# Optimization experiments

Hardware: AMD Instinct MI355X
Metric: run time of the kernel (lower is better)

## Reference

```python
import jax, jax.numpy as jnp
import numpy as np


def _pair_indices(num_emb):
    # pair (i, j), i != j; torch builds pair vector = concat(emb[j], emb[i])
    ii, jj = np.meshgrid(np.arange(num_emb), np.arange(num_emb), indexing='ij')
    mask = ii != jj
    return jnp.asarray(ii[mask]), jnp.asarray(jj[mask])


def setup_inputs() -> dict:
    key = jax.random.key(0)
    ks = jax.random.split(key, 8)
    B, n_way, n_shot, n_query, F = 64, 2, 6, 16, 512
    s = 0.02
    return {
        'x_shot_feat': jax.random.normal(ks[0], (B * n_way * n_shot, F), jnp.float32),
        'x_query_feat': jax.random.normal(ks[1], (B * n_query, F), jnp.float32),
        'Wg1': jax.random.normal(ks[2], (2 * F, F), jnp.float32) * s,
        'bg1': jnp.zeros((F,), jnp.float32),
        'Wg2': jax.random.normal(ks[3], (F, F), jnp.float32) * s,
        'bg2': jnp.zeros((F,), jnp.float32),
        'Wf1': jax.random.normal(ks[4], (F, F), jnp.float32) * s,
        'bf1': jnp.zeros((F,), jnp.float32),
        'Wf2': jax.random.normal(ks[5], (F, 1), jnp.float32) * s,
        'bf2': jnp.zeros((1,), jnp.float32),
        'batch_size': B, 'n_way': n_way, 'n_shot': n_shot, 'n_query': n_query,
    }


def reference(x_shot_feat, x_query_feat, Wg1, bg1, Wg2, bg2, Wf1, bf1, Wf2, bf2,
              batch_size, n_way, n_shot, n_query):
    F = x_shot_feat.shape[-1]
    num_emb = n_shot + 1
    x_shot = x_shot_feat.reshape(batch_size, n_way, n_shot, F)
    pos, neg = x_shot[:, 0], x_shot[:, 1]          # [B, n_shot, F]
    q = x_query_feat.reshape(batch_size, n_query, F)

    # emb: [B, Q, way=2, num_emb, F]  (support set + the single query appended)
    shot = jnp.stack([pos, neg], axis=1)           # [B, 2, n_shot, F]
    shot_b = jnp.broadcast_to(shot[:, None], (batch_size, n_query, 2, n_shot, F))
    q_b = jnp.broadcast_to(q[:, :, None, None, :], (batch_size, n_query, 2, 1, F))
    emb = jnp.concatenate([shot_b, q_b], axis=3)   # [B, Q, 2, num_emb, F]

    idx_i, idx_j = _pair_indices(num_emb)          # P = num_emb^2 - num_emb
    # pair(i,j) = concat(emb[j], emb[i])  (matches torch expand order)
    pairs = jnp.concatenate([emb[..., idx_j, :], emb[..., idx_i, :]], axis=-1)  # [B,Q,2,P,2F]

    g = jax.nn.relu(pairs @ Wg1 + bg1)
    g = jax.nn.relu(g @ Wg2 + bg2)                 # [B, Q, 2, P, F]
    s = jnp.sum(g, axis=3)                         # [B, Q, 2, F]
    logit = jax.nn.relu(s @ Wf1 + bf1) @ Wf2 + bf2 # [B, Q, 2, 1]
    return logit[..., 0]                           # [B, Q, n_way]
```

## Files before the change

### kernel.cpp

```cpp
#include <hip/hip_runtime.h>
#include <stdint.h>

typedef _Float16 f16x8 __attribute__((ext_vector_type(8)));
typedef float f32x4 __attribute__((ext_vector_type(4)));

__device__ __forceinline__ void gload16(const void* g, void* l) {
  __builtin_amdgcn_global_load_lds((const __attribute__((address_space(1))) void*)g,
                                   (__attribute__((address_space(3))) void*)l,
                                   16, 0, 0);
}

__device__ __forceinline__ void maprow_ss(int gr, int& rowU, int& rowV, bool& ok) {
  int g = gr >> 5, p = gr & 31;
  ok = (p < 30);
  int i = p / 5, jj = p % 5;
  int j = jj + (jj >= i);
  rowU = g * 6 + j;
  rowV = g * 6 + i;
  if (!ok) { rowU = 0; rowV = 0; }
}

__device__ __forceinline__ void maprow_sq(int gr, int& rowU, int& rowV) {
  int h = gr / 12, p = gr % 12;
  int b = h >> 5, q = (h >> 1) & 15, wv = h & 1;
  int sbase = (b * 2 + wv) * 6;
  int qrow = 768 + b * 16 + q;
  if (p < 6) { rowU = qrow; rowV = sbase + p; }
  else       { rowU = sbase + (p - 6); rowV = qrow; }
}

__device__ __forceinline__ f16x8 cvt8h(float4 a, float4 b) {
  f16x8 o;
  o[0] = (_Float16)a.x; o[1] = (_Float16)a.y; o[2] = (_Float16)a.z; o[3] = (_Float16)a.w;
  o[4] = (_Float16)b.x; o[5] = (_Float16)b.y; o[6] = (_Float16)b.z; o[7] = (_Float16)b.w;
  return o;
}

__global__ void convert_t(const float* __restrict__ Wg1, const float* __restrict__ Wg2,
                          const float* __restrict__ Wf1, const float* __restrict__ bf2,
                          _Float16* __restrict__ Wg1T, _Float16* __restrict__ Wg2T,
                          _Float16* __restrict__ Wf1T, float* __restrict__ out) {
  int tt = blockIdx.x * 256 + threadIdx.x;
  if (tt < 2048) out[tt] = bf2[0];
  const float* src;
  _Float16* dst;
  int c, k0, scol, srow0;
  if (tt < 65536) {
    c = tt & 1023; k0 = (tt >> 10) << 3;
    dst = Wg1T + (size_t)c * 512 + k0;
    if (c < 512) { src = Wg1; scol = c; srow0 = k0; }
    else         { src = Wg1; scol = c - 512; srow0 = 512 + k0; }
  } else if (tt < 98304) {
    int t2 = tt - 65536;
    c = t2 & 511; k0 = (t2 >> 9) << 3;
    dst = Wg2T + (size_t)c * 512 + k0;
    src = Wg2; scol = c; srow0 = k0;
  } else {
    int t3 = tt - 98304;
    c = t3 & 511; k0 = (t3 >> 9) << 3;
    dst = Wf1T + (size_t)c * 512 + k0;
    src = Wf1; scol = c; srow0 = k0;
  }
  f16x8 o;
#pragma unroll
  for (int i = 0; i < 8; i++)
    o[i] = (_Float16)src[(size_t)(srow0 + i) * 512 + scol];
  *(f16x8*)dst = o;
}

__global__ __launch_bounds__(256, 2) void gemm1_fused(
    const float* __restrict__ xs, const float* __restrict__ xq,
    const _Float16* __restrict__ BT, const float* __restrict__ bg1,
    _Float16* __restrict__ UVh) {
  __shared__ __align__(16) char smem[16384];

  int bid = blockIdx.x;
  { int q = gridDim.x >> 3; bid = (bid & 7) * q + (bid >> 3); }
  const int tm = bid >> 4;
  const int tn = bid & 15;
  const int t = threadIdx.x, w = t >> 6, l = t & 63;
  const int wm = (w >> 1) << 5, wn = (w & 1) << 5;
  const int lr = l & 15, lg = l >> 4;

  const int rl0 = t >> 2, c = t & 3;
  const int wchunk = c ^ ((rl0 >> 2) & 3);
  const int gr0 = tm * 64 + rl0;
  const float* x0 = ((gr0 < 768) ? xs + (size_t)gr0 * 512 : xq + (size_t)(gr0 - 768) * 512) + c * 8;

  const int kch = ((t & 3) ^ ((t >> 4) & 3)) * 8;
  const _Float16* Bg = BT + (size_t)(tn * 64 + rl0) * 512 + kch;

  _Float16* As_base = (_Float16*)smem;
  char*     Bs_base = smem + 8192;

  f32x4 acc[2][2];
#pragma unroll
  for (int m = 0; m < 2; m++)
#pragma unroll
    for (int n = 0; n < 2; n++) acc[m][n] = (f32x4){0.f, 0.f, 0.f, 0.f};
  const int rchunk = (lg ^ (lr >> 2)) * 8;

  gload16(Bg, Bs_base + t * 16);
  {
    float4 a0 = *(const float4*)(x0), a1 = *(const float4*)(x0 + 4);
    *(f16x8*)(As_base + rl0 * 32 + wchunk * 8) = cvt8h(a0, a1);
  }
  __syncthreads();

  int cur = 0;
  for (int it = 0; it < 15; ++it) {
    const int nxt = cur ^ 1;
    const int kn = (it + 1) * 32;
    gload16(Bg + kn, Bs_base + nxt * 4096 + t * 16);
    float4 a0 = *(const float4*)(x0 + kn), a1 = *(const float4*)(x0 + kn + 4);
    {
      _Float16* As = As_base + cur * 2048;
      _Float16* Bs = (_Float16*)(Bs_base + cur * 4096);
      f16x8 fa[2], fb[2];
#pragma unroll
      for (int m = 0; m < 2; m++)
        fa[m] = *(const f16x8*)(As + (wm + m * 16 + lr) * 32 + rchunk);
#pragma unroll
      for (int n = 0; n < 2; n++)
        fb[n] = *(const f16x8*)(Bs + (wn + n * 16 + lr) * 32 + rchunk);
#pragma unroll
      for (int m = 0; m < 2; m++)
#pragma unroll
        for (int n = 0; n < 2; n++)
          acc[m][n] = __builtin_amdgcn_mfma_f32_16x16x32_f16(fa[m], fb[n], acc[m][n], 0, 0, 0);
    }
    *(f16x8*)(As_base + nxt * 2048 + rl0 * 32 + wchunk * 8) = cvt8h(a0, a1);
    __syncthreads();
    cur = nxt;
  }
  {
    _Float16* As = As_base + cur * 2048;
    _Float16* Bs = (_Float16*)(Bs_base + cur * 4096);
    f16x8 fa[2], fb[2];
#pragma unroll
    for (int m = 0; m < 2; m++)
      fa[m] = *(const f16x8*)(As + (wm + m * 16 + lr) * 32 + rchunk);
#pragma unroll
    for (int n = 0; n < 2; n++)
      fb[n] = *(const f16x8*)(Bs + (wn + n * 16 + lr) * 32 + rchunk);
#pragma unroll
    for (int m = 0; m < 2; m++)
#pragma unroll
      for (int n = 0; n < 2; n++)
        acc[m][n] = __builtin_amdgcn_mfma_f32_16x16x32_f16(fa[m], fb[n], acc[m][n], 0, 0, 0);
  }

#pragma unroll
  for (int m = 0; m < 2; m++)
#pragma unroll
    for (int n = 0; n < 2; n++) {
      int col = tn * 64 + wn + n * 16 + lr;
      float bv = (col >= 512) ? bg1[col - 512] : 0.0f;
#pragma unroll
      for (int reg = 0; reg < 4; reg++) {
        int row = tm * 64 + wm + m * 16 + lg * 4 + reg;
        UVh[(size_t)row * 1024 + col] = (_Float16)(acc[m][n][reg] + bv);
      }
    }
}

__global__ __launch_bounds__(256, 2) void gemm2_fused(
    const _Float16* __restrict__ UVh,
    const _Float16* __restrict__ BT, const float* __restrict__ bg2,
    float* __restrict__ outSS, float* __restrict__ outSQ) {
  __shared__ __align__(16) char smem[24576];

  int bid = blockIdx.x;
  { int q = gridDim.x >> 3; bid = (bid & 7) * q + (bid >> 3); }
  const int t = threadIdx.x, w = t >> 6, l = t & 63;
  const int lr = l & 15, lg = l >> 4;
  const int rl = t >> 2, c = t & 3;
  const int wchunk = c ^ ((t >> 4) & 3);
  const int kch = ((t & 3) ^ ((t >> 4) & 3)) * 8;
  const int rchunk = (lg ^ (lr >> 2)) * 8;
  const f16x8 zz = {};
  char* Bsb = smem + 16384;

  if (bid < 2048) {
    const int tile = bid >> 3, tn = bid & 7;
    const int wm = (w >> 1) * 48, wn = (w & 1) << 5;

    int rU0, rV0, rU1 = 0, rV1 = 0;
    maprow_sq(tile * 96 + rl, rU0, rV0);
    if (t < 128) maprow_sq(tile * 96 + 64 + rl, rU1, rV1);
    const _Float16* u0p = UVh + (size_t)rU0 * 1024 + c * 8;
    const _Float16* v0p = UVh + (size_t)rV0 * 1024 + 512 + c * 8;
    const _Float16* u1p = UVh + (size_t)rU1 * 1024 + c * 8;
    const _Float16* v1p = UVh + (size_t)rV1 * 1024 + 512 + c * 8;
    const _Float16* Bg = BT + (size_t)(tn * 64 + rl) * 512 + kch;

    f32x4 acc[3][2];
#pragma unroll
    for (int m = 0; m < 3; m++)
#pragma unroll
      for (int n = 0; n < 2; n++) acc[m][n] = (f32x4){0.f, 0.f, 0.f, 0.f};

    {
      f16x8 u0 = *(const f16x8*)(u0p), v0 = *(const f16x8*)(v0p);
      *(f16x8*)((_Float16*)smem + rl * 32 + wchunk * 8) =
          __builtin_elementwise_max(u0 + v0, zz);
      if (t < 128) {
        f16x8 u1 = *(const f16x8*)(u1p), v1 = *(const f16x8*)(v1p);
        *(f16x8*)((_Float16*)smem + (64 + rl) * 32 + wchunk * 8) =
            __builtin_elementwise_max(u1 + v1, zz);
      }
    }
    gload16(Bg, Bsb + t * 16);
    __syncthreads();

    int cur = 0;
    for (int it = 0; it < 15; ++it) {
      const int nxt = cur ^ 1;
      const int kn = (it + 1) * 32;
      gload16(Bg + kn, Bsb + nxt * 4096 + t * 16);
      f16x8 u0 = *(const f16x8*)(u0p + kn), v0 = *(const f16x8*)(v0p + kn);
      f16x8 u1, v1;
      if (t < 128) { u1 = *(const f16x8*)(u1p + kn); v1 = *(const f16x8*)(v1p + kn); }
      {
        _Float16* As = (_Float16*)(smem + cur * 6144);
        _Float16* Bs = (_Float16*)(Bsb + cur * 4096);
        f16x8 fa[3], fb[2];
#pragma unroll
        for (int m = 0; m < 3; m++)
          fa[m] = *(const f16x8*)(As + (wm + m * 16 + lr) * 32 + rchunk);
#pragma unroll
        for (int n = 0; n < 2; n++)
          fb[n] = *(const f16x8*)(Bs + (wn + n * 16 + lr) * 32 + rchunk);
#pragma unroll
        for (int m = 0; m < 3; m++)
#pragma unroll
          for (int n = 0; n < 2; n++)
            acc[m][n] = __builtin_amdgcn_mfma_f32_16x16x32_f16(fa[m], fb[n], acc[m][n], 0, 0, 0);
      }
      {
        _Float16* Aw = (_Float16*)(smem + nxt * 6144);
        *(f16x8*)(Aw + rl * 32 + wchunk * 8) = __builtin_elementwise_max(u0 + v0, zz);
        if (t < 128)
          *(f16x8*)(Aw + (64 + rl) * 32 + wchunk * 8) = __builtin_elementwise_max(u1 + v1, zz);
      }
      __syncthreads();
      cur = nxt;
    }
    {
      _Float16* As = (_Float16*)(smem + cur * 6144);
      _Float16* Bs = (_Float16*)(Bsb + cur * 4096);
      f16x8 fa[3], fb[2];
#pragma unroll
      for (int m = 0; m < 3; m++)
        fa[m] = *(const f16x8*)(As + (wm + m * 16 + lr) * 32 + rchunk);
#pragma unroll
      for (int n = 0; n < 2; n++)
        fb[n] = *(const f16x8*)(Bs + (wn + n * 16 + lr) * 32 + rchunk);
#pragma unroll
      for (int m = 0; m < 3; m++)
#pragma unroll
        for (int n = 0; n < 2; n++)
          acc[m][n] = __builtin_amdgcn_mfma_f32_16x16x32_f16(fa[m], fb[n], acc[m][n], 0, 0, 0);
    }
    __syncthreads();

    float* scr = (float*)smem + w * 192;
#pragma unroll
    for (int n = 0; n < 2; n++) {
      int col = tn * 64 + wn + n * 16 + lr;
      float bv = bg2[col];
#pragma unroll
      for (int m = 0; m < 3; m++) {
        float s = 0.0f;
#pragma unroll
        for (int reg = 0; reg < 4; reg++)
          s += fmaxf(acc[m][n][reg] + bv, 0.0f);
        scr[(4 * m + lg) * 16 + lr] = s;
      }
#pragma unroll
      for (int g = 0; g < 4; g++) {
        float vs = scr[(3 * g) * 16 + lr] + scr[(3 * g + 1) * 16 + lr] +
                   scr[(3 * g + 2) * 16 + lr];
        if (l < 16) {
          int hh = tile * 8 + ((wm == 48) ? 4 : 0) + g;
          outSQ[(size_t)hh * 512 + col] = vs;
        }
      }
    }
  } else {
    const int sbid = bid - 2048;
    const int tm = sbid >> 3, tn = sbid & 7;
    const int wm = (w >> 1) << 6, wn = (w & 1) << 5;

    int rU0, rV0, rU1, rV1; bool ok0, ok1;
    maprow_ss(tm * 128 + rl, rU0, rV0, ok0);
    maprow_ss(tm * 128 + rl + 64, rU1, rV1, ok1);
    const _Float16* u0p = UVh + (size_t)rU0 * 1024 + c * 8;
    const _Float16* v0p = UVh + (size_t)rV0 * 1024 + 512 + c * 8;
    const _Float16* u1p = UVh + (size_t)rU1 * 1024 + c * 8;
    const _Float16* v1p = UVh + (size_t)rV1 * 1024 + 512 + c * 8;
    const _Float16* Bg = BT + (size_t)(tn * 64 + rl) * 512 + kch;

    f32x4 acc[4][2];
#pragma unroll
    for (int m = 0; m < 4; m++)
#pragma unroll
      for (int n = 0; n < 2; n++) acc[m][n] = (f32x4){0.f, 0.f, 0.f, 0.f};

    {
      f16x8 u0 = *(const f16x8*)(u0p), v0 = *(const f16x8*)(v0p);
      f16x8 u1 = *(const f16x8*)(u1p), v1 = *(const f16x8*)(v1p);
      f16x8 o0 = ok0 ? __builtin_elementwise_max(u0 + v0, zz) : zz;
      f16x8 o1 = ok1 ? __builtin_elementwise_max(u1 + v1, zz) : zz;
      *(f16x8*)((_Float16*)smem + rl * 32 + wchunk * 8) = o0;
      *(f16x8*)((_Float16*)smem + (rl + 64) * 32 + wchunk * 8) = o1;
    }
    gload16(Bg, Bsb + t * 16);
    __syncthreads();

    int cur = 0;
    for (int it = 0; it < 15; ++it) {
      const int nxt = cur ^ 1;
      const int kn = (it + 1) * 32;
      gload16(Bg + kn, Bsb + nxt * 4096 + t * 16);
      f16x8 u0 = *(const f16x8*)(u0p + kn), v0 = *(const f16x8*)(v0p + kn);
      f16x8 u1 = *(const f16x8*)(u1p + kn), v1 = *(const f16x8*)(v1p + kn);
      {
        _Float16* As = (_Float16*)(smem + cur * 8192);
        _Float16* Bs = (_Float16*)(Bsb + cur * 4096);
        f16x8 fa[4], fb[2];
#pragma unroll
        for (int m = 0; m < 4; m++)
          fa[m] = *(const f16x8*)(As + (wm + m * 16 + lr) * 32 + rchunk);
#pragma unroll
        for (int n = 0; n < 2; n++)
          fb[n] = *(const f16x8*)(Bs + (wn + n * 16 + lr) * 32 + rchunk);
#pragma unroll
        for (int m = 0; m < 4; m++)
#pragma unroll
          for (int n = 0; n < 2; n++)
            acc[m][n] = __builtin_amdgcn_mfma_f32_16x16x32_f16(fa[m], fb[n], acc[m][n], 0, 0, 0);
      }
      {
        f16x8 o0 = ok0 ? __builtin_elementwise_max(u0 + v0, zz) : zz;
        f16x8 o1 = ok1 ? __builtin_elementwise_max(u1 + v1, zz) : zz;
        _Float16* Aw = (_Float16*)(smem + nxt * 8192);
        *(f16x8*)(Aw + rl * 32 + wchunk * 8) = o0;
        *(f16x8*)(Aw + (rl + 64) * 32 + wchunk * 8) = o1;
      }
      __syncthreads();
      cur = nxt;
    }
    {
      _Float16* As = (_Float16*)(smem + cur * 8192);
      _Float16* Bs = (_Float16*)(Bsb + cur * 4096);
      f16x8 fa[4], fb[2];
#pragma unroll
      for (int m = 0; m < 4; m++)
        fa[m] = *(const f16x8*)(As + (wm + m * 16 + lr) * 32 + rchunk);
#pragma unroll
      for (int n = 0; n < 2; n++)
        fb[n] = *(const f16x8*)(Bs + (wn + n * 16 + lr) * 32 + rchunk);
#pragma unroll
      for (int m = 0; m < 4; m++)
#pragma unroll
        for (int n = 0; n < 2; n++)
          acc[m][n] = __builtin_amdgcn_mfma_f32_16x16x32_f16(fa[m], fb[n], acc[m][n], 0, 0, 0);
    }

#pragma unroll
    for (int pair = 0; pair < 2; pair++) {
#pragma unroll
      for (int n = 0; n < 2; n++) {
        int col = tn * 64 + wn + n * 16 + lr;
        float bv = bg2[col];
        float s = 0.0f;
#pragma unroll
        for (int mh = 0; mh < 2; mh++) {
          int m = pair * 2 + mh;
#pragma unroll
          for (int reg = 0; reg < 4; reg++) {
            bool ok = (mh == 0) || (lg * 4 + reg < 14);
            float v = fmaxf(acc[m][n][reg] + bv, 0.0f);
            s += ok ? v : 0.0f;
          }
        }
        s += __shfl_xor(s, 16);
        s += __shfl_xor(s, 32);
        if (l < 16) {
          int g = (wm >> 5) + pair;
          outSS[(size_t)(tm * 4 + g) * 512 + col] = s;
        }
      }
    }
  }
}

__global__ __launch_bounds__(256, 2) void gemm3_fused(
    const float* __restrict__ SS, const float* __restrict__ SQ,
    const _Float16* __restrict__ BT, const float* __restrict__ bf1,
    const float* __restrict__ Wf2, float* __restrict__ out) {
  __shared__ __align__(16) char smem[16384];

  int bid = blockIdx.x;
  { int q = gridDim.x >> 3; bid = (bid & 7) * q + (bid >> 3); }
  const int tm = bid >> 3;
  const int tn = bid & 7;
  const int t = threadIdx.x, w = t >> 6, l = t & 63;
  const int wm = (w >> 1) << 5, wn = (w & 1) << 5;
  const int lr = l & 15, lg = l >> 4;

  const int rl0 = t >> 2, c = t & 3;
  const int wchunk = c ^ ((rl0 >> 2) & 3);
  const int gr0 = tm * 64 + rl0;
  const int ss0 = (gr0 >> 5) * 2 + (gr0 & 1);
  const float* s0p = SS + (size_t)ss0 * 512 + c * 8;
  const float* q0p = SQ + (size_t)gr0 * 512 + c * 8;

  const int kch = ((t & 3) ^ ((t >> 4) & 3)) * 8;
  const _Float16* Bg = BT + (size_t)(tn * 64 + rl0) * 512 + kch;

  _Float16* As_base = (_Float16*)smem;
  char*     Bs_base = smem + 8192;

  f32x4 acc[2][2];
#pragma unroll
  for (int m = 0; m < 2; m++)
#pragma unroll
    for (int n = 0; n < 2; n++) acc[m][n] = (f32x4){0.f, 0.f, 0.f, 0.f};
  const int rchunk = (lg ^ (lr >> 2)) * 8;

#define BUILD_S(o, a0, a1, b0, b1)                                           \
  {                                                                          \
    o[0] = (_Float16)(a0.x + b0.x); o[1] = (_Float16)(a0.y + b0.y);          \
    o[2] = (_Float16)(a0.z + b0.z); o[3] = (_Float16)(a0.w + b0.w);          \
    o[4] = (_Float16)(a1.x + b1.x); o[5] = (_Float16)(a1.y + b1.y);          \
    o[6] = (_Float16)(a1.z + b1.z); o[7] = (_Float16)(a1.w + b1.w);          \
  }

  gload16(Bg, Bs_base + t * 16);
  {
    float4 a0 = *(const float4*)(s0p), a1 = *(const float4*)(s0p + 4);
    float4 b0 = *(const float4*)(q0p), b1 = *(const float4*)(q0p + 4);
    f16x8 o0;
    BUILD_S(o0, a0, a1, b0, b1);
    *(f16x8*)(As_base + rl0 * 32 + wchunk * 8) = o0;
  }
  __syncthreads();

  int cur = 0;
  for (int it = 0; it < 15; ++it) {
    const int nxt = cur ^ 1;
    const int kn = (it + 1) * 32;
    gload16(Bg + kn, Bs_base + nxt * 4096 + t * 16);
    float4 a0 = *(const float4*)(s0p + kn), a1 = *(const float4*)(s0p + kn + 4);
    float4 b0 = *(const float4*)(q0p + kn), b1 = *(const float4*)(q0p + kn + 4);
    {
      _Float16* As = As_base + cur * 2048;
      _Float16* Bs = (_Float16*)(Bs_base + cur * 4096);
      f16x8 fa[2], fb[2];
#pragma unroll
      for (int m = 0; m < 2; m++)
        fa[m] = *(const f16x8*)(As + (wm + m * 16 + lr) * 32 + rchunk);
#pragma unroll
      for (int n = 0; n < 2; n++)
        fb[n] = *(const f16x8*)(Bs + (wn + n * 16 + lr) * 32 + rchunk);
#pragma unroll
      for (int m = 0; m < 2; m++)
#pragma unroll
        for (int n = 0; n < 2; n++)
          acc[m][n] = __builtin_amdgcn_mfma_f32_16x16x32_f16(fa[m], fb[n], acc[m][n], 0, 0, 0);
    }
    {
      f16x8 o0;
      BUILD_S(o0, a0, a1, b0, b1);
      *(f16x8*)(As_base + nxt * 2048 + rl0 * 32 + wchunk * 8) = o0;
    }
    __syncthreads();
    cur = nxt;
  }
  {
    _Float16* As = As_base + cur * 2048;
    _Float16* Bs = (_Float16*)(Bs_base + cur * 4096);
    f16x8 fa[2], fb[2];
#pragma unroll
    for (int m = 0; m < 2; m++)
      fa[m] = *(const f16x8*)(As + (wm + m * 16 + lr) * 32 + rchunk);
#pragma unroll
    for (int n = 0; n < 2; n++)
      fb[n] = *(const f16x8*)(Bs + (wn + n * 16 + lr) * 32 + rchunk);
#pragma unroll
    for (int m = 0; m < 2; m++)
#pragma unroll
      for (int n = 0; n < 2; n++)
        acc[m][n] = __builtin_amdgcn_mfma_f32_16x16x32_f16(fa[m], fb[n], acc[m][n], 0, 0, 0);
  }

  float bf1v[2], wf2v[2];
#pragma unroll
  for (int n = 0; n < 2; n++) {
    int col = tn * 64 + wn + n * 16 + lr;
    bf1v[n] = bf1[col];
    wf2v[n] = Wf2[col];
  }
#pragma unroll
  for (int m = 0; m < 2; m++) {
#pragma unroll
    for (int reg = 0; reg < 4; reg++) {
      float p = 0.0f;
#pragma unroll
      for (int n = 0; n < 2; n++)
        p += fmaxf(acc[m][n][reg] + bf1v[n], 0.0f) * wf2v[n];
      p += __shfl_xor(p, 1);
      p += __shfl_xor(p, 2);
      p += __shfl_xor(p, 4);
      p += __shfl_xor(p, 8);
      if (lr == 0) {
        int row = tm * 64 + wm + m * 16 + lg * 4 + reg;
        atomicAdd(&out[row], p);
      }
    }
  }
#undef BUILD_S
}

extern "C" void kernel_launch(void* const* d_in, const int* in_sizes, int n_in,
                              void* d_out, int out_size, void* d_ws, size_t ws_size,
                              hipStream_t stream) {
  const float* xs  = (const float*)d_in[0];
  const float* xq  = (const float*)d_in[1];
  const float* Wg1 = (const float*)d_in[2];
  const float* bg1 = (const float*)d_in[3];
  const float* Wg2 = (const float*)d_in[4];
  const float* bg2 = (const float*)d_in[5];
  const float* Wf1 = (const float*)d_in[6];
  const float* bf1 = (const float*)d_in[7];
  const float* Wf2 = (const float*)d_in[8];
  const float* bf2 = (const float*)d_in[9];
  float* out = (float*)d_out;

  char* ws = (char*)d_ws;
  _Float16* Wg1T = (_Float16*)(ws);
  _Float16* Wg2T = (_Float16*)(ws + 1048576);
  _Float16* Wf1T = (_Float16*)(ws + 1572864);
  _Float16* UVh  = (_Float16*)(ws + 2097152);
  float*    SSs  = (float*)(ws + 5767168);
  float*    SQs  = (float*)(ws + 6029312);

  convert_t<<<512, 256, 0, stream>>>(Wg1, Wg2, Wf1, bf2, Wg1T, Wg2T, Wf1T, out);
  gemm1_fused<<<448, 256, 0, stream>>>(xs, xq, Wg1T, bg1, UVh);
  gemm2_fused<<<2304, 256, 0, stream>>>(UVh, Wg2T, bg2, SSs, SQs);
  gemm3_fused<<<256, 256, 0, stream>>>(SSs, SQs, Wf1T, bf1, Wf2, out);
}
```

Before: 64.14 us.

## Widen gemm2 tiles to 128 columns with 512-thread blocks

Doubles the N-tile width of the fused second GEMM from 64 to 128 columns and runs it with 8 waves per 512-thread block, halving the grid. Each block now builds its relu(U+V) A-tile once per 128 output columns instead of once per 64, so the pair-gather and add work and the UVh reads are cut in half. The B shared buffer doubles and the block shrinks to one per CU by launch bounds, which may lower latency hiding and occupancy.

```diff
diff --git a/kernel.cpp b/kernel.cpp
--- a/kernel.cpp
+++ b/kernel.cpp
@@ -164,35 +164,34 @@
     }
 }
 
-__global__ __launch_bounds__(256, 2) void gemm2_fused(
+__global__ __launch_bounds__(512, 1) void gemm2_fused(
     const _Float16* __restrict__ UVh,
     const _Float16* __restrict__ BT, const float* __restrict__ bg2,
     float* __restrict__ outSS, float* __restrict__ outSQ) {
-  __shared__ __align__(16) char smem[24576];
+  __shared__ __align__(16) char smem[32768];
 
   int bid = blockIdx.x;
   { int q = gridDim.x >> 3; bid = (bid & 7) * q + (bid >> 3); }
   const int t = threadIdx.x, w = t >> 6, l = t & 63;
   const int lr = l & 15, lg = l >> 4;
   const int rl = t >> 2, c = t & 3;
-  const int wchunk = c ^ ((t >> 4) & 3);
+  const int wchunk = c ^ ((rl >> 2) & 3);
   const int kch = ((t & 3) ^ ((t >> 4) & 3)) * 8;
   const int rchunk = (lg ^ (lr >> 2)) * 8;
   const f16x8 zz = {};
   char* Bsb = smem + 16384;
 
-  if (bid < 2048) {
-    const int tile = bid >> 3, tn = bid & 7;
-    const int wm = (w >> 1) * 48, wn = (w & 1) << 5;
-
-    int rU0, rV0, rU1 = 0, rV1 = 0;
-    maprow_sq(tile * 96 + rl, rU0, rV0);
-    if (t < 128) maprow_sq(tile * 96 + 64 + rl, rU1, rV1);
+  if (bid < 1024) {
+    const int tile = bid >> 2, tn = bid & 3;
+    const int wm = (w >> 2) * 48;
+    const int wn = (w & 3) << 5;
+    const bool st = (t < 384);
+
+    int rU0 = 0, rV0 = 0;
+    if (st) maprow_sq(tile * 96 + rl, rU0, rV0);
     const _Float16* u0p = UVh + (size_t)rU0 * 1024 + c * 8;
     const _Float16* v0p = UVh + (size_t)rV0 * 1024 + 512 + c * 8;
-    const _Float16* u1p = UVh + (size_t)rU1 * 1024 + c * 8;
-    const _Float16* v1p = UVh + (size_t)rV1 * 1024 + 512 + c * 8;
-    const _Float16* Bg = BT + (size_t)(tn * 64 + rl) * 512 + kch;
+    const _Float16* Bg = BT + (size_t)(tn * 128 + rl) * 512 + kch;
 
     f32x4 acc[3][2];
 #pragma unroll
@@ -200,15 +199,10 @@
 #pragma unroll
       for (int n = 0; n < 2; n++) acc[m][n] = (f32x4){0.f, 0.f, 0.f, 0.f};
 
-    {
+    if (st) {
       f16x8 u0 = *(const f16x8*)(u0p), v0 = *(const f16x8*)(v0p);
       *(f16x8*)((_Float16*)smem + rl * 32 + wchunk * 8) =
           __builtin_elementwise_max(u0 + v0, zz);
-      if (t < 128) {
-        f16x8 u1 = *(const f16x8*)(u1p), v1 = *(const f16x8*)(v1p);
-        *(f16x8*)((_Float16*)smem + (64 + rl) * 32 + wchunk * 8) =
-            __builtin_elementwise_max(u1 + v1, zz);
-      }
     }
     gload16(Bg, Bsb + t * 16);
     __syncthreads();
@@ -217,13 +211,12 @@
     for (int it = 0; it < 15; ++it) {
       const int nxt = cur ^ 1;
       const int kn = (it + 1) * 32;
-      gload16(Bg + kn, Bsb + nxt * 4096 + t * 16);
-      f16x8 u0 = *(const f16x8*)(u0p + kn), v0 = *(const f16x8*)(v0p + kn);
-      f16x8 u1, v1;
-      if (t < 128) { u1 = *(const f16x8*)(u1p + kn); v1 = *(const f16x8*)(v1p + kn); }
+      gload16(Bg + kn, Bsb + nxt * 8192 + t * 16);
+      f16x8 u0, v0;
+      if (st) { u0 = *(const f16x8*)(u0p + kn); v0 = *(const f16x8*)(v0p + kn); }
       {
         _Float16* As = (_Float16*)(smem + cur * 6144);
-        _Float16* Bs = (_Float16*)(Bsb + cur * 4096);
+        _Float16* Bs = (_Float16*)(Bsb + cur * 8192);
         f16x8 fa[3], fb[2];
 #pragma unroll
         for (int m = 0; m < 3; m++)
@@ -237,18 +230,16 @@
           for (int n = 0; n < 2; n++)
             acc[m][n] = __builtin_amdgcn_mfma_f32_16x16x32_f16(fa[m], fb[n], acc[m][n], 0, 0, 0);
       }
-      {
+      if (st) {
         _Float16* Aw = (_Float16*)(smem + nxt * 6144);
         *(f16x8*)(Aw + rl * 32 + wchunk * 8) = __builtin_elementwise_max(u0 + v0, zz);
-        if (t < 128)
-          *(f16x8*)(Aw + (64 + rl) * 32 + wchunk * 8) = __builtin_elementwise_max(u1 + v1, zz);
       }
       __syncthreads();
       cur = nxt;
     }
     {
       _Float16* As = (_Float16*)(smem + cur * 6144);
-      _Float16* Bs = (_Float16*)(Bsb + cur * 4096);
+      _Float16* Bs = (_Float16*)(Bsb + cur * 8192);
       f16x8 fa[3], fb[2];
 #pragma unroll
       for (int m = 0; m < 3; m++)
@@ -267,7 +258,7 @@
     float* scr = (float*)smem + w * 192;
 #pragma unroll
     for (int n = 0; n < 2; n++) {
-      int col = tn * 64 + wn + n * 16 + lr;
+      int col = tn * 128 + wn + n * 16 + lr;
       float bv = bg2[col];
 #pragma unroll
       for (int m = 0; m < 3; m++) {
@@ -288,18 +279,16 @@
       }
     }
   } else {
-    const int sbid = bid - 2048;
-    const int tm = sbid >> 3, tn = sbid & 7;
-    const int wm = (w >> 1) << 6, wn = (w & 1) << 5;
-
-    int rU0, rV0, rU1, rV1; bool ok0, ok1;
+    const int sbid = bid - 1024;
+    const int tm = sbid >> 2, tn = sbid & 3;
+    const int wm = (w >> 2) << 6;
+    const int wn = (w & 3) << 5;
+
+    int rU0, rV0; bool ok0;
     maprow_ss(tm * 128 + rl, rU0, rV0, ok0);
-    maprow_ss(tm * 128 + rl + 64, rU1, rV1, ok1);
     const _Float16* u0p = UVh + (size_t)rU0 * 1024 + c * 8;
     const _Float16* v0p = UVh + (size_t)rV0 * 1024 + 512 + c * 8;
-    const _Float16* u1p = UVh + (size_t)rU1 * 1024 + c * 8;
-    const _Float16* v1p = UVh + (size_t)rV1 * 1024 + 512 + c * 8;
-    const _Float16* Bg = BT + (size_t)(tn * 64 + rl) * 512 + kch;
+    const _Float16* Bg = BT + (size_t)(tn * 128 + rl) * 512 + kch;
 
     f32x4 acc[4][2];
 #pragma unroll
@@ -309,11 +298,8 @@
 
     {
       f16x8 u0 = *(const f16x8*)(u0p), v0 = *(const f16x8*)(v0p);
-      f16x8 u1 = *(const f16x8*)(u1p), v1 = *(const f16x8*)(v1p);
       f16x8 o0 = ok0 ? __builtin_elementwise_max(u0 + v0, zz) : zz;
-      f16x8 o1 = ok1 ? __builtin_elementwise_max(u1 + v1, zz) : zz;
       *(f16x8*)((_Float16*)smem + rl * 32 + wchunk * 8) = o0;
-      *(f16x8*)((_Float16*)smem + (rl + 64) * 32 + wchunk * 8) = o1;
     }
     gload16(Bg, Bsb + t * 16);
     __syncthreads();
@@ -322,12 +308,11 @@
     for (int it = 0; it < 15; ++it) {
       const int nxt = cur ^ 1;
       const int kn = (it + 1) * 32;
-      gload16(Bg + kn, Bsb + nxt * 4096 + t * 16);
+      gload16(Bg + kn, Bsb + nxt * 8192 + t * 16);
       f16x8 u0 = *(const f16x8*)(u0p + kn), v0 = *(const f16x8*)(v0p + kn);
-      f16x8 u1 = *(const f16x8*)(u1p + kn), v1 = *(const f16x8*)(v1p + kn);
       {
         _Float16* As = (_Float16*)(smem + cur * 8192);
-        _Float16* Bs = (_Float16*)(Bsb + cur * 4096);
+        _Float16* Bs = (_Float16*)(Bsb + cur * 8192);
         f16x8 fa[4], fb[2];
 #pragma unroll
         for (int m = 0; m < 4; m++)
@@ -343,17 +328,15 @@
       }
       {
         f16x8 o0 = ok0 ? __builtin_elementwise_max(u0 + v0, zz) : zz;
-        f16x8 o1 = ok1 ? __builtin_elementwise_max(u1 + v1, zz) : zz;
         _Float16* Aw = (_Float16*)(smem + nxt * 8192);
         *(f16x8*)(Aw + rl * 32 + wchunk * 8) = o0;
-        *(f16x8*)(Aw + (rl + 64) * 32 + wchunk * 8) = o1;
       }
       __syncthreads();
       cur = nxt;
     }
     {
       _Float16* As = (_Float16*)(smem + cur * 8192);
-      _Float16* Bs = (_Float16*)(Bsb + cur * 4096);
+      _Float16* Bs = (_Float16*)(Bsb + cur * 8192);
       f16x8 fa[4], fb[2];
 #pragma unroll
       for (int m = 0; m < 4; m++)
@@ -372,7 +355,7 @@
     for (int pair = 0; pair < 2; pair++) {
 #pragma unroll
       for (int n = 0; n < 2; n++) {
-        int col = tn * 64 + wn + n * 16 + lr;
+        int col = tn * 128 + wn + n * 16 + lr;
         float bv = bg2[col];
         float s = 0.0f;
 #pragma unroll
@@ -549,6 +532,6 @@
 
   convert_t<<<512, 256, 0, stream>>>(Wg1, Wg2, Wf1, bf2, Wg1T, Wg2T, Wf1T, out);
   gemm1_fused<<<448, 256, 0, stream>>>(xs, xq, Wg1T, bg1, UVh);
-  gemm2_fused<<<2304, 256, 0, stream>>>(UVh, Wg2T, bg2, SSs, SQs);
+  gemm2_fused<<<1152, 512, 0, stream>>>(UVh, Wg2T, bg2, SSs, SQs);
   gemm3_fused<<<256, 256, 0, stream>>>(SSs, SQs, Wf1T, bf1, Wf2, out);
 }
```

Result: no change. 63.91 us (-0.4%).
